# Performance work log

Hardware: AMD Instinct MI355X
Metric: run time of the kernel (lower is better)

## Reference

```python
import jax, jax.numpy as jnp
import numpy as np

DIM = 256
NUM_HEADS = 8
HEAD_DIM = DIM // NUM_HEADS


def setup_inputs() -> dict:
    key = jax.random.key(0)
    k_x, k_wq, k_bq, k_wp, k_bp = jax.random.split(key, 5)
    B, C, H, W = 2, DIM, 48, 48
    x = jax.random.normal(k_x, (B, C, H, W), dtype=jnp.float32)
    # 1x1 convs are pointwise matmuls: store weights as [out, in]
    w_qkv = jax.random.normal(k_wq, (3 * C, C), dtype=jnp.float32) * (1.0 / np.sqrt(C))
    b_qkv = jax.random.normal(k_bq, (3 * C,), dtype=jnp.float32) * 0.01
    w_proj = jax.random.normal(k_wp, (C, C), dtype=jnp.float32) * (1.0 / np.sqrt(C))
    b_proj = jax.random.normal(k_bp, (C,), dtype=jnp.float32) * 0.01
    return {"x": x, "w_qkv": w_qkv, "b_qkv": b_qkv, "w_proj": w_proj, "b_proj": b_proj}


def reference(x, w_qkv, b_qkv, w_proj, b_proj):
    B, C, H, W = x.shape
    N = H * W
    # qkv 1x1 conv -> pointwise channel matmul
    qkv = jnp.einsum('bchw,oc->bohw', x, w_qkv) + b_qkv[None, :, None, None]
    q, k, v = jnp.split(qkv, 3, axis=1)  # each [B, C, H, W]
    q = q.reshape(B, NUM_HEADS, HEAD_DIM, N)
    k = k.reshape(B, NUM_HEADS, HEAD_DIM, N)
    v = v.reshape(B, NUM_HEADS, HEAD_DIM, N)
    scale = 1.0 / (HEAD_DIM ** 0.5)
    attn = jnp.einsum('bhdn,bhdm->bhnm', q, k) * scale  # [B, H, N, N]
    attn = jax.nn.softmax(attn, axis=-1)
    out = jnp.einsum('bhnm,bhdm->bhdn', attn, v)  # [B, heads, head_dim, N]
    out = out.reshape(B, C, H, W)
    out = jnp.einsum('bchw,oc->bohw', out, w_proj) + b_proj[None, :, None, None]
    return out + x
```

## Files before the change

### kernel.cpp

```cpp
#include <hip/hip_runtime.h>
#include <math.h>

#define C_DIM 256
#define NH 8
#define HD 32
#define NPIX 2304
#define NGRP 144
#define TK 64
#define TPB 18

typedef __attribute__((ext_vector_type(8))) short bf16x8;
typedef __attribute__((ext_vector_type(4))) float f32x4;

#define OFF_XT  0u
#define OFF_Q   1179648u
#define OFF_K   2359296u
#define OFF_V   3538944u
#define OFF_OT  4718592u
#define OFF_WQ  5898240u
#define OFF_WP  6094848u
#define OFF_F32 6160384u

__device__ __forceinline__ unsigned short f2b(float f) {
    union { float f; unsigned int u; } c; c.f = f;
    unsigned int u = c.u + 0x7FFFu + ((c.u >> 16) & 1u);
    return (unsigned short)(u >> 16);
}
__device__ __forceinline__ unsigned int pk2(float lo, float hi) {
    union { float f; unsigned int u; } a, b;
    a.f = lo; b.f = hi;
    return __builtin_amdgcn_perm(b.u + 0x8000u, a.u + 0x8000u, 0x07060302u);
}

__global__ __launch_bounds__(256) void prep_all(
        const float* __restrict__ x, const float* __restrict__ wqkv,
        const float* __restrict__ wproj, unsigned short* __restrict__ wsp)
{
    __shared__ unsigned short t_s[64][72];
    const int tid = threadIdx.x;
    const int u = blockIdx.x;
    if (u < 288) {
        const int n0 = (u % 36) * 64, cb = (u / 36) % 4, b = u / 144;
        const int c0 = cb * 64;
        const int nl = tid & 63, cq = tid >> 6;
        #pragma unroll
        for (int p = 0; p < 8; ++p) {
            const int c = p * 8 + cq * 2;
            const float f0 = x[((size_t)b * C_DIM + c0 + c) * NPIX + n0 + nl];
            const float f1 = x[((size_t)b * C_DIM + c0 + c + 1) * NPIX + n0 + nl];
            *(unsigned int*)&t_s[nl][c] = pk2(f0, f1);
        }
        __syncthreads();
        unsigned short* xT = wsp + OFF_XT;
        const int row = tid >> 2, jq = tid & 3;
        #pragma unroll
        for (int hh = 0; hh < 2; ++hh) {
            const int jl = jq * 2 + hh;
            const int jg = cb * 8 + jl;
            const int ngrp = (u % 36) * 4 + (row >> 4);
            unsigned short* dst = xT + (((size_t)b * NGRP + ngrp) * 32 + jg) * 128 + (row & 15) * 8;
            *(uint4*)dst = *(uint4*)&t_s[row][jl * 8];
        }
    } else {
        const int t = (u - 288) * 256 + tid;
        const float* src; unsigned short* dst;
        if (t < 24576) {
            const int m = t >> 5, j = t & 31;
            src = wqkv + ((size_t)m * C_DIM + j * 8);
            dst = wsp + OFF_WQ + ((size_t)((m >> 4) * 32 + j) * 16 + (m & 15)) * 8;
        } else {
            const int t2 = t - 24576, m = t2 >> 5, j = t2 & 31;
            src = wproj + ((size_t)m * C_DIM + j * 8);
            dst = wsp + OFF_WP + ((size_t)((m >> 4) * 32 + j) * 16 + (m & 15)) * 8;
        }
        const float4 f0 = *(const float4*)src, f1 = *(const float4*)(src + 4);
        *(uint4*)dst = make_uint4(pk2(f0.x, f0.y), pk2(f0.z, f0.w),
                                  pk2(f1.x, f1.y), pk2(f1.z, f1.w));
    }
}

__global__ __launch_bounds__(256, 2) void qkv_gemm(
        const unsigned short* __restrict__ xT, const unsigned short* __restrict__ wq,
        const float* __restrict__ bias,
        unsigned short* __restrict__ Qg, unsigned short* __restrict__ Kg,
        unsigned short* __restrict__ Vg)
{
    __shared__ unsigned short eplds[4][2560];
    const int tid = threadIdx.x, wv = tid >> 6, lane = tid & 63;
    const int l15 = lane & 15, quad = lane >> 4;
    const int n0 = blockIdx.x * 256, my = blockIdx.y, b = blockIdx.z;
    const int nw = n0 + wv * 64;

    bf16x8 af[2][8];
    #pragma unroll
    for (int mt = 0; mt < 2; ++mt)
        #pragma unroll
        for (int kc = 0; kc < 8; ++kc)
            af[mt][kc] = *(const bf16x8*)(wq +
                ((size_t)((my * 2 + mt) * 32 + kc * 4 + quad) * 16 + l15) * 8);

    f32x4 acc[2][4];
    #pragma unroll
    for (int mt = 0; mt < 2; ++mt)
        #pragma unroll
        for (int s = 0; s < 4; ++s) acc[mt][s] = (f32x4){0.f, 0.f, 0.f, 0.f};

    #pragma unroll
    for (int sub = 0; sub < 4; ++sub) {
        const int ngrp = (nw + sub * 16) >> 4;
        const unsigned short* bp = xT + ((size_t)b * NGRP + ngrp) * 32 * 128;
        #pragma unroll
        for (int kc = 0; kc < 8; ++kc) {
            const bf16x8 bf = *(const bf16x8*)(bp + (size_t)(kc * 4 + quad) * 128 + l15 * 8);
            acc[0][sub] = __builtin_amdgcn_mfma_f32_16x16x32_bf16(af[0][kc], bf, acc[0][sub], 0, 0, 0);
            acc[1][sub] = __builtin_amdgcn_mfma_f32_16x16x32_bf16(af[1][kc], bf, acc[1][sub], 0, 0, 0);
        }
    }

    const int which = my >> 3;
    const int h = my & 7, bh = b * NH + h;
    float4 b4[2];
    b4[0] = *(const float4*)(bias + my * 32 + quad * 4);
    b4[1] = *(const float4*)(bias + my * 32 + 16 + quad * 4);
    unsigned short* wl = eplds[wv];

    if (which < 2) {
        const float sc = (which == 0) ? 0.25503484f : 1.0f;
        #pragma unroll
        for (int mt = 0; mt < 2; ++mt)
            #pragma unroll
            for (int sub = 0; sub < 4; ++sub) {
                const float v0 = (acc[mt][sub][0] + b4[mt].x) * sc;
                const float v1 = (acc[mt][sub][1] + b4[mt].y) * sc;
                const float v2 = (acc[mt][sub][2] + b4[mt].z) * sc;
                const float v3 = (acc[mt][sub][3] + b4[mt].w) * sc;
                *(uint2*)&wl[(sub * 16 + l15) * 40 + mt * 16 + quad * 4] =
                    make_uint2(pk2(v0, v1), pk2(v2, v3));
            }
        unsigned short* dst = ((which == 0) ? Qg : Kg)
                            + ((size_t)bh * NPIX + nw + lane) * HD;
        #pragma unroll
        for (int i = 0; i < 4; ++i)
            *((uint4*)dst + i) = *(uint4*)&wl[lane * 40 + i * 8];
    } else {
        #pragma unroll
        for (int mt = 0; mt < 2; ++mt)
            #pragma unroll
            for (int sub = 0; sub < 4; ++sub) {
                wl[(mt * 16 + quad * 4 + 0) * 72 + sub * 16 + l15] = f2b(acc[mt][sub][0] + b4[mt].x);
                wl[(mt * 16 + quad * 4 + 1) * 72 + sub * 16 + l15] = f2b(acc[mt][sub][1] + b4[mt].y);
                wl[(mt * 16 + quad * 4 + 2) * 72 + sub * 16 + l15] = f2b(acc[mt][sub][2] + b4[mt].z);
                wl[(mt * 16 + quad * 4 + 3) * 72 + sub * 16 + l15] = f2b(acc[mt][sub][3] + b4[mt].w);
            }
        const int row = lane >> 1, seg = (lane & 1) * 32;
        unsigned short* dst = Vg + ((size_t)bh * HD + row) * NPIX + nw + seg;
        #pragma unroll
        for (int i = 0; i < 4; ++i)
            *((uint4*)dst + i) = *(uint4*)&wl[row * 72 + seg + i * 8];
    }
}

__global__ __launch_bounds__(256, 4) void attn_kernel(
        const unsigned short* __restrict__ Qg, const unsigned short* __restrict__ Kg,
        const unsigned short* __restrict__ Vg,
        float* __restrict__ OtP, float* __restrict__ lsumP)
{
    __shared__ unsigned short k_s[2][TK][40];
    __shared__ unsigned short v_s[2][HD][76];
    __shared__ unsigned short p_s[4][16][76];

    const int tid  = threadIdx.x;
    const int wv   = tid >> 6;
    const int lane = tid & 63;
    const int l15  = lane & 15;
    const int quad = lane >> 4;
    const int bh   = blockIdx.x;
    const int q0   = blockIdx.y * 64;
    const int sp   = blockIdx.z;
    const int t0   = sp * TPB;

    const unsigned short* Qh = Qg + (size_t)bh * NPIX * HD;
    const unsigned short* Kh = Kg + (size_t)bh * NPIX * HD;
    const unsigned short* Vh = Vg + (size_t)bh * HD * NPIX;

    const bf16x8 q_frag = *(const bf16x8*)(Qh + (size_t)(q0 + wv * 16 + l15) * HD + quad * 8);

    const int kr = tid >> 2, kc = (tid & 3) * 8;
    const int vd = tid >> 3, vc = (tid & 7) * 8;

    uint4 kreg = *(const uint4*)(Kh + (size_t)(t0 * TK + kr) * HD + kc);
    uint4 vreg = *(const uint4*)(Vh + (size_t)vd * NPIX + t0 * TK + vc);
    *(uint4*)&k_s[0][kr][kc] = kreg;
    *(uint4*)&v_s[0][vd][vc] = vreg;

    f32x4 o0 = {0.f, 0.f, 0.f, 0.f};
    f32x4 o1 = {0.f, 0.f, 0.f, 0.f};
    float lsum = 0.f;

    for (int t = 0; t < TPB; ++t) {
        const int cur = t & 1;
        if (t + 1 < TPB) {
            const int k0 = (t0 + t + 1) * TK;
            kreg = *(const uint4*)(Kh + (size_t)(k0 + kr) * HD + kc);
            vreg = *(const uint4*)(Vh + (size_t)vd * NPIX + k0 + vc);
        }
        __syncthreads();

        f32x4 s[4];
        #pragma unroll
        for (int kg = 0; kg < 4; ++kg) {
            const bf16x8 kf = *(const bf16x8*)&k_s[cur][kg * 16 + l15][quad * 8];
            s[kg] = __builtin_amdgcn_mfma_f32_16x16x32_bf16(kf, q_frag,
                        (f32x4){0.f, 0.f, 0.f, 0.f}, 0, 0, 0);
        }

        #pragma unroll
        for (int kg = 0; kg < 4; ++kg) {
            const float p0 = exp2f(s[kg][0]);
            const float p1 = exp2f(s[kg][1]);
            const float p2 = exp2f(s[kg][2]);
            const float p3 = exp2f(s[kg][3]);
            lsum += (p0 + p1) + (p2 + p3);
            *(uint2*)&p_s[wv][l15][kg * 16 + quad * 4] =
                make_uint2(pk2(p0, p1), pk2(p2, p3));
        }

        #pragma unroll
        for (int kc2 = 0; kc2 < 2; ++kc2) {
            const bf16x8 pf  = *(const bf16x8*)&p_s[wv][l15][kc2 * 32 + quad * 8];
            const bf16x8 vf0 = *(const bf16x8*)&v_s[cur][l15][kc2 * 32 + quad * 8];
            const bf16x8 vf1 = *(const bf16x8*)&v_s[cur][16 + l15][kc2 * 32 + quad * 8];
            o0 = __builtin_amdgcn_mfma_f32_16x16x32_bf16(vf0, pf, o0, 0, 0, 0);
            o1 = __builtin_amdgcn_mfma_f32_16x16x32_bf16(vf1, pf, o1, 0, 0, 0);
        }

        if (t + 1 < TPB) {
            *(uint4*)&k_s[cur ^ 1][kr][kc] = kreg;
            *(uint4*)&v_s[cur ^ 1][vd][vc] = vreg;
        }
    }

    lsum += __shfl_xor(lsum, 16, 64);
    lsum += __shfl_xor(lsum, 32, 64);

    __syncthreads();
    float* pp = (float*)&p_s[wv][0][0];
    #pragma unroll
    for (int r = 0; r < 4; ++r) {
        pp[l15 * 36 + quad * 4 + r]      = o0[r];
        pp[l15 * 36 + 16 + quad * 4 + r] = o1[r];
    }
    if (quad == 0)
        lsumP[((size_t)sp * 16 + bh) * NPIX + q0 + wv * 16 + l15] = lsum;
    __syncthreads();
    const int q = lane >> 2, off = (lane & 3) * 8;
    float* dst = OtP + (((size_t)sp * 16 + bh) * NPIX + q0 + wv * 16 + q) * 32 + off;
    *(float4*)dst       = *(float4*)&pp[q * 36 + off];
    *((float4*)dst + 1) = *(float4*)&pp[q * 36 + off + 4];
}

__global__ __launch_bounds__(256) void norm_kernel(
        const float* __restrict__ OtP, const float* __restrict__ lsumP,
        unsigned short* __restrict__ OtT)
{
    const int bh = blockIdx.x;
    const int q = blockIdx.y * 256 + threadIdx.x;
    const float* pa = OtP + ((size_t)bh * NPIX + q) * 32;
    const float* pb = OtP + ((size_t)(16 + bh) * NPIX + q) * 32;
    const float inv = 1.f / (lsumP[(size_t)bh * NPIX + q] +
                             lsumP[(size_t)(16 + bh) * NPIX + q]);
    const int b = bh >> 3, h = bh & 7;
    unsigned short* cell = OtT + (((size_t)b * NGRP + (q >> 4)) * 32 + h * 4) * 128
                         + (q & 15) * 8;
    #pragma unroll
    for (int jq = 0; jq < 4; ++jq) {
        const float4 a0 = *(const float4*)(pa + jq * 8);
        const float4 a1 = *(const float4*)(pa + jq * 8 + 4);
        const float4 b0 = *(const float4*)(pb + jq * 8);
        const float4 b1 = *(const float4*)(pb + jq * 8 + 4);
        const float o0 = (a0.x + b0.x) * inv, o1 = (a0.y + b0.y) * inv;
        const float o2 = (a0.z + b0.z) * inv, o3 = (a0.w + b0.w) * inv;
        const float o4 = (a1.x + b1.x) * inv, o5 = (a1.y + b1.y) * inv;
        const float o6 = (a1.z + b1.z) * inv, o7 = (a1.w + b1.w) * inv;
        *(uint4*)(cell + jq * 128) = make_uint4(pk2(o0, o1), pk2(o2, o3),
                                                pk2(o4, o5), pk2(o6, o7));
    }
}

__global__ __launch_bounds__(256) void proj_gemm(
        const unsigned short* __restrict__ OtT, const unsigned short* __restrict__ wp,
        const float* __restrict__ bias, const float* __restrict__ x,
        float* __restrict__ out)
{
    __shared__ float plds[4][576];
    const int tid = threadIdx.x, wv = tid >> 6, lane = tid & 63;
    const int l15 = lane & 15, quad = lane >> 4;
    const int n0 = blockIdx.x * 128, my = blockIdx.y, b = blockIdx.z;
    const int nw = n0 + wv * 32;

    bf16x8 af[8];
    #pragma unroll
    for (int kc = 0; kc < 8; ++kc)
        af[kc] = *(const bf16x8*)(wp + ((size_t)(my * 32 + kc * 4 + quad) * 16 + l15) * 8);

    f32x4 acc[2];
    acc[0] = (f32x4){0.f, 0.f, 0.f, 0.f};
    acc[1] = (f32x4){0.f, 0.f, 0.f, 0.f};

    #pragma unroll
    for (int sub = 0; sub < 2; ++sub) {
        const int ngrp = (nw >> 4) + sub;
        const unsigned short* bp = OtT + ((size_t)b * NGRP + ngrp) * 32 * 128;
        #pragma unroll
        for (int kc = 0; kc < 8; ++kc) {
            const bf16x8 bf = *(const bf16x8*)(bp + (size_t)(kc * 4 + quad) * 128 + l15 * 8);
            acc[sub] = __builtin_amdgcn_mfma_f32_16x16x32_bf16(af[kc], bf, acc[sub], 0, 0, 0);
        }
    }

    float* wl = plds[wv];
    #pragma unroll
    for (int sub = 0; sub < 2; ++sub) {
        wl[(quad * 4 + 0) * 36 + sub * 16 + l15] = acc[sub][0];
        wl[(quad * 4 + 1) * 36 + sub * 16 + l15] = acc[sub][1];
        wl[(quad * 4 + 2) * 36 + sub * 16 + l15] = acc[sub][2];
        wl[(quad * 4 + 3) * 36 + sub * 16 + l15] = acc[sub][3];
    }
    __syncthreads();
    const int m0 = my * 16;
    #pragma unroll
    for (int p = 0; p < 2; ++p) {
        const int row = p * 8 + (lane >> 3), cn = (lane & 7) * 4;
        const int c = m0 + row;
        const size_t idx = ((size_t)b * C_DIM + c) * NPIX + nw + cn;
        const f32x4 v = *(const f32x4*)&wl[row * 36 + cn];
        const f32x4 r = *(const f32x4*)(x + idx);
        const float bv = bias[c];
        f32x4 o;
        o[0] = v[0] + bv + r[0]; o[1] = v[1] + bv + r[1];
        o[2] = v[2] + bv + r[2]; o[3] = v[3] + bv + r[3];
        *(f32x4*)(out + idx) = o;
    }
}

extern "C" void kernel_launch(void* const* d_in, const int* in_sizes, int n_in,
                              void* d_out, int out_size, void* d_ws, size_t ws_size,
                              hipStream_t stream)
{
    const float* x      = (const float*)d_in[0];
    const float* w_qkv  = (const float*)d_in[1];
    const float* b_qkv  = (const float*)d_in[2];
    const float* w_proj = (const float*)d_in[3];
    const float* b_proj = (const float*)d_in[4];
    float* out = (float*)d_out;

    unsigned short* ws = (unsigned short*)d_ws;
    unsigned short* xT  = ws + OFF_XT;
    unsigned short* Qg  = ws + OFF_Q;
    unsigned short* Kg  = ws + OFF_K;
    unsigned short* Vg  = ws + OFF_V;
    unsigned short* OtT = ws + OFF_OT;
    unsigned short* wq  = ws + OFF_WQ;
    unsigned short* wp  = ws + OFF_WP;
    float* fws   = (float*)(ws + OFF_F32);
    float* OtP   = fws;
    float* lsumP = fws + 4718592;

    prep_all<<<dim3(416), 256, 0, stream>>>(x, w_qkv, w_proj, ws);
    qkv_gemm<<<dim3(9, 24, 2), 256, 0, stream>>>(xT, wq, b_qkv, Qg, Kg, Vg);
    attn_kernel<<<dim3(16, 36, 2), 256, 0, stream>>>(Qg, Kg, Vg, OtP, lsumP);
    norm_kernel<<<dim3(16, 9), 256, 0, stream>>>(OtP, lsumP, OtT);
    proj_gemm<<<dim3(18, 16, 2), 256, 0, stream>>>(OtT, wp, b_proj, x, out);
}
```

Measured before the change: 122.6 us.

## Restructure attention: per-wave direct K/V fragment loads, 32 queries per wave, 4-way key split

The attention kernel stops staging K and V through double-buffered shared memory with block barriers. Each wave now loads MFMA fragments directly from global memory, and V gets a new fragment-major layout written by the QKV GEMM so those loads are contiguous. Each wave now covers 32 queries, so every loaded K/V fragment feeds twice as many MFMAs. The key dimension is split four ways instead of two, and the normalization kernel sums four partials. This removes barriers and LDS traffic in the inner loop, but doubles the fp32 partial-output writes and reads and depends on caches to serve the repeated K/V loads.

```diff
diff --git a/kernel.cpp b/kernel.cpp
--- a/kernel.cpp
+++ b/kernel.cpp
@@ -6,8 +6,8 @@
 #define HD 32
 #define NPIX 2304
 #define NGRP 144
-#define TK 64
-#define TPB 18
+#define NSP 4
+#define ATPB 9
 
 typedef __attribute__((ext_vector_type(8))) short bf16x8;
 typedef __attribute__((ext_vector_type(4))) float f32x4;
@@ -83,7 +83,7 @@
         const unsigned short* __restrict__ xT, const unsigned short* __restrict__ wq,
         const float* __restrict__ bias,
         unsigned short* __restrict__ Qg, unsigned short* __restrict__ Kg,
-        unsigned short* __restrict__ Vg)
+        unsigned short* __restrict__ Vfm)
 {
     __shared__ unsigned short eplds[4][2560];
     const int tid = threadIdx.x, wv = tid >> 6, lane = tid & 63;
@@ -152,111 +152,102 @@
                 wl[(mt * 16 + quad * 4 + 2) * 72 + sub * 16 + l15] = f2b(acc[mt][sub][2] + b4[mt].z);
                 wl[(mt * 16 + quad * 4 + 3) * 72 + sub * 16 + l15] = f2b(acc[mt][sub][3] + b4[mt].w);
             }
-        const int row = lane >> 1, seg = (lane & 1) * 32;
-        unsigned short* dst = Vg + ((size_t)bh * HD + row) * NPIX + nw + seg;
+        const int row = lane >> 1;
+        const int half = lane & 1;
+        unsigned short* dst = Vfm + (((size_t)bh * 72 + (nw >> 5) + half) * 2 + (row >> 4)) * 512
+                            + (row & 15) * 32;
         #pragma unroll
         for (int i = 0; i < 4; ++i)
-            *((uint4*)dst + i) = *(uint4*)&wl[row * 72 + seg + i * 8];
+            *((uint4*)dst + i) = *(uint4*)&wl[row * 72 + half * 32 + i * 8];
     }
 }
 
 __global__ __launch_bounds__(256, 4) void attn_kernel(
         const unsigned short* __restrict__ Qg, const unsigned short* __restrict__ Kg,
-        const unsigned short* __restrict__ Vg,
+        const unsigned short* __restrict__ Vfm,
         float* __restrict__ OtP, float* __restrict__ lsumP)
 {
-    __shared__ unsigned short k_s[2][TK][40];
-    __shared__ unsigned short v_s[2][HD][76];
-    __shared__ unsigned short p_s[4][16][76];
-
-    const int tid  = threadIdx.x;
-    const int wv   = tid >> 6;
-    const int lane = tid & 63;
-    const int l15  = lane & 15;
-    const int quad = lane >> 4;
-    const int bh   = blockIdx.x;
-    const int q0   = blockIdx.y * 64;
-    const int sp   = blockIdx.z;
-    const int t0   = sp * TPB;
+    __shared__ unsigned short ps_all[4][2304];
+    const int tid = threadIdx.x, wv = tid >> 6, lane = tid & 63;
+    const int l15 = lane & 15, quad = lane >> 4;
+    const int bh = blockIdx.x, qb = blockIdx.y, sp = blockIdx.z;
+    const int tqb = qb * 128 + wv * 32;
 
     const unsigned short* Qh = Qg + (size_t)bh * NPIX * HD;
     const unsigned short* Kh = Kg + (size_t)bh * NPIX * HD;
-    const unsigned short* Vh = Vg + (size_t)bh * HD * NPIX;
-
-    const bf16x8 q_frag = *(const bf16x8*)(Qh + (size_t)(q0 + wv * 16 + l15) * HD + quad * 8);
-
-    const int kr = tid >> 2, kc = (tid & 3) * 8;
-    const int vd = tid >> 3, vc = (tid & 7) * 8;
-
-    uint4 kreg = *(const uint4*)(Kh + (size_t)(t0 * TK + kr) * HD + kc);
-    uint4 vreg = *(const uint4*)(Vh + (size_t)vd * NPIX + t0 * TK + vc);
-    *(uint4*)&k_s[0][kr][kc] = kreg;
-    *(uint4*)&v_s[0][vd][vc] = vreg;
-
-    f32x4 o0 = {0.f, 0.f, 0.f, 0.f};
-    f32x4 o1 = {0.f, 0.f, 0.f, 0.f};
-    float lsum = 0.f;
-
-    for (int t = 0; t < TPB; ++t) {
-        const int cur = t & 1;
-        if (t + 1 < TPB) {
-            const int k0 = (t0 + t + 1) * TK;
-            kreg = *(const uint4*)(Kh + (size_t)(k0 + kr) * HD + kc);
-            vreg = *(const uint4*)(Vh + (size_t)vd * NPIX + k0 + vc);
-        }
-        __syncthreads();
-
-        f32x4 s[4];
+    const unsigned short* Vb = Vfm + (size_t)bh * 73728;
+
+    const bf16x8 qf0 = *(const bf16x8*)(Qh + (size_t)(tqb + l15) * HD + quad * 8);
+    const bf16x8 qf1 = *(const bf16x8*)(Qh + (size_t)(tqb + 16 + l15) * HD + quad * 8);
+
+    unsigned short* ps = ps_all[wv];
+    f32x4 o[2][2];
+    #pragma unroll
+    for (int i = 0; i < 2; ++i) { o[i][0] = (f32x4){0,0,0,0}; o[i][1] = (f32x4){0,0,0,0}; }
+    float ls0 = 0.f, ls1 = 0.f;
+
+    for (int t = 0; t < ATPB; ++t) {
+        const int k0 = (sp * ATPB + t) * 64;
+        bf16x8 kf[4];
+        #pragma unroll
+        for (int kg = 0; kg < 4; ++kg)
+            kf[kg] = *(const bf16x8*)(Kh + (size_t)(k0 + kg * 16 + l15) * HD + quad * 8);
+        f32x4 s0[4], s1[4];
         #pragma unroll
         for (int kg = 0; kg < 4; ++kg) {
-            const bf16x8 kf = *(const bf16x8*)&k_s[cur][kg * 16 + l15][quad * 8];
-            s[kg] = __builtin_amdgcn_mfma_f32_16x16x32_bf16(kf, q_frag,
-                        (f32x4){0.f, 0.f, 0.f, 0.f}, 0, 0, 0);
-        }
-
+            s0[kg] = __builtin_amdgcn_mfma_f32_16x16x32_bf16(kf[kg], qf0, (f32x4){0,0,0,0}, 0, 0, 0);
+            s1[kg] = __builtin_amdgcn_mfma_f32_16x16x32_bf16(kf[kg], qf1, (f32x4){0,0,0,0}, 0, 0, 0);
+        }
         #pragma unroll
         for (int kg = 0; kg < 4; ++kg) {
-            const float p0 = exp2f(s[kg][0]);
-            const float p1 = exp2f(s[kg][1]);
-            const float p2 = exp2f(s[kg][2]);
-            const float p3 = exp2f(s[kg][3]);
-            lsum += (p0 + p1) + (p2 + p3);
-            *(uint2*)&p_s[wv][l15][kg * 16 + quad * 4] =
-                make_uint2(pk2(p0, p1), pk2(p2, p3));
-        }
-
+            const float a0 = exp2f(s0[kg][0]), a1 = exp2f(s0[kg][1]);
+            const float a2 = exp2f(s0[kg][2]), a3 = exp2f(s0[kg][3]);
+            ls0 += (a0 + a1) + (a2 + a3);
+            *(uint2*)&ps[(size_t)l15 * 72 + kg * 16 + quad * 4] =
+                make_uint2(pk2(a0, a1), pk2(a2, a3));
+            const float b0 = exp2f(s1[kg][0]), b1 = exp2f(s1[kg][1]);
+            const float b2 = exp2f(s1[kg][2]), b3 = exp2f(s1[kg][3]);
+            ls1 += (b0 + b1) + (b2 + b3);
+            *(uint2*)&ps[(size_t)(16 + l15) * 72 + kg * 16 + quad * 4] =
+                make_uint2(pk2(b0, b1), pk2(b2, b3));
+        }
         #pragma unroll
         for (int kc2 = 0; kc2 < 2; ++kc2) {
-            const bf16x8 pf  = *(const bf16x8*)&p_s[wv][l15][kc2 * 32 + quad * 8];
-            const bf16x8 vf0 = *(const bf16x8*)&v_s[cur][l15][kc2 * 32 + quad * 8];
-            const bf16x8 vf1 = *(const bf16x8*)&v_s[cur][16 + l15][kc2 * 32 + quad * 8];
-            o0 = __builtin_amdgcn_mfma_f32_16x16x32_bf16(vf0, pf, o0, 0, 0, 0);
-            o1 = __builtin_amdgcn_mfma_f32_16x16x32_bf16(vf1, pf, o1, 0, 0, 0);
-        }
-
-        if (t + 1 < TPB) {
-            *(uint4*)&k_s[cur ^ 1][kr][kc] = kreg;
-            *(uint4*)&v_s[cur ^ 1][vd][vc] = vreg;
-        }
-    }
-
-    lsum += __shfl_xor(lsum, 16, 64);
-    lsum += __shfl_xor(lsum, 32, 64);
-
-    __syncthreads();
-    float* pp = (float*)&p_s[wv][0][0];
-    #pragma unroll
-    for (int r = 0; r < 4; ++r) {
-        pp[l15 * 36 + quad * 4 + r]      = o0[r];
-        pp[l15 * 36 + 16 + quad * 4 + r] = o1[r];
-    }
-    if (quad == 0)
-        lsumP[((size_t)sp * 16 + bh) * NPIX + q0 + wv * 16 + l15] = lsum;
-    __syncthreads();
-    const int q = lane >> 2, off = (lane & 3) * 8;
-    float* dst = OtP + (((size_t)sp * 16 + bh) * NPIX + q0 + wv * 16 + q) * 32 + off;
-    *(float4*)dst       = *(float4*)&pp[q * 36 + off];
-    *((float4*)dst + 1) = *(float4*)&pp[q * 36 + off + 4];
+            const int kb = (k0 >> 5) + kc2;
+            const bf16x8 vf0 = *(const bf16x8*)(Vb + ((size_t)kb * 2 + 0) * 512 + l15 * 32 + quad * 8);
+            const bf16x8 vf1 = *(const bf16x8*)(Vb + ((size_t)kb * 2 + 1) * 512 + l15 * 32 + quad * 8);
+            const bf16x8 pf0 = *(const bf16x8*)&ps[(size_t)l15 * 72 + kc2 * 32 + quad * 8];
+            const bf16x8 pf1 = *(const bf16x8*)&ps[(size_t)(16 + l15) * 72 + kc2 * 32 + quad * 8];
+            o[0][0] = __builtin_amdgcn_mfma_f32_16x16x32_bf16(vf0, pf0, o[0][0], 0, 0, 0);
+            o[0][1] = __builtin_amdgcn_mfma_f32_16x16x32_bf16(vf1, pf0, o[0][1], 0, 0, 0);
+            o[1][0] = __builtin_amdgcn_mfma_f32_16x16x32_bf16(vf0, pf1, o[1][0], 0, 0, 0);
+            o[1][1] = __builtin_amdgcn_mfma_f32_16x16x32_bf16(vf1, pf1, o[1][1], 0, 0, 0);
+        }
+    }
+
+    ls0 += __shfl_xor(ls0, 16, 64); ls0 += __shfl_xor(ls0, 32, 64);
+    ls1 += __shfl_xor(ls1, 16, 64); ls1 += __shfl_xor(ls1, 32, 64);
+    if (quad == 0) {
+        lsumP[((size_t)sp * 16 + bh) * NPIX + tqb + l15]      = ls0;
+        lsumP[((size_t)sp * 16 + bh) * NPIX + tqb + 16 + l15] = ls1;
+    }
+
+    float* tl = (float*)ps;
+    #pragma unroll
+    for (int qs = 0; qs < 2; ++qs) {
+        __builtin_amdgcn_s_waitcnt(0);
+        #pragma unroll
+        for (int r = 0; r < 4; ++r) {
+            tl[l15 * 36 + quad * 4 + r]      = o[qs][0][r];
+            tl[l15 * 36 + 16 + quad * 4 + r] = o[qs][1][r];
+        }
+        __builtin_amdgcn_s_waitcnt(0);
+        const int qq = lane >> 2, j = lane & 3;
+        float* dst = OtP + (((size_t)sp * 16 + bh) * NPIX + tqb + qs * 16 + qq) * 32 + j * 8;
+        *(float4*)dst       = *(float4*)&tl[qq * 36 + j * 8];
+        *((float4*)dst + 1) = *(float4*)&tl[qq * 36 + j * 8 + 4];
+        __builtin_amdgcn_s_waitcnt(0);
+    }
 }
 
 __global__ __launch_bounds__(256) void norm_kernel(
@@ -265,25 +256,25 @@
 {
     const int bh = blockIdx.x;
     const int q = blockIdx.y * 256 + threadIdx.x;
-    const float* pa = OtP + ((size_t)bh * NPIX + q) * 32;
-    const float* pb = OtP + ((size_t)(16 + bh) * NPIX + q) * 32;
+    const float* p0 = OtP + ((size_t)bh * NPIX + q) * 32;
+    const float* p1 = OtP + ((size_t)(16 + bh) * NPIX + q) * 32;
+    const float* p2 = OtP + ((size_t)(32 + bh) * NPIX + q) * 32;
+    const float* p3 = OtP + ((size_t)(48 + bh) * NPIX + q) * 32;
     const float inv = 1.f / (lsumP[(size_t)bh * NPIX + q] +
-                             lsumP[(size_t)(16 + bh) * NPIX + q]);
+                             lsumP[(size_t)(16 + bh) * NPIX + q] +
+                             lsumP[(size_t)(32 + bh) * NPIX + q] +
+                             lsumP[(size_t)(48 + bh) * NPIX + q]);
     const int b = bh >> 3, h = bh & 7;
     unsigned short* cell = OtT + (((size_t)b * NGRP + (q >> 4)) * 32 + h * 4) * 128
                          + (q & 15) * 8;
     #pragma unroll
     for (int jq = 0; jq < 4; ++jq) {
-        const float4 a0 = *(const float4*)(pa + jq * 8);
-        const float4 a1 = *(const float4*)(pa + jq * 8 + 4);
-        const float4 b0 = *(const float4*)(pb + jq * 8);
-        const float4 b1 = *(const float4*)(pb + jq * 8 + 4);
-        const float o0 = (a0.x + b0.x) * inv, o1 = (a0.y + b0.y) * inv;
-        const float o2 = (a0.z + b0.z) * inv, o3 = (a0.w + b0.w) * inv;
-        const float o4 = (a1.x + b1.x) * inv, o5 = (a1.y + b1.y) * inv;
-        const float o6 = (a1.z + b1.z) * inv, o7 = (a1.w + b1.w) * inv;
-        *(uint4*)(cell + jq * 128) = make_uint4(pk2(o0, o1), pk2(o2, o3),
-                                                pk2(o4, o5), pk2(o6, o7));
+        float v[8];
+        #pragma unroll
+        for (int e = 0; e < 8; ++e)
+            v[e] = (p0[jq * 8 + e] + p1[jq * 8 + e] + p2[jq * 8 + e] + p3[jq * 8 + e]) * inv;
+        *(uint4*)(cell + jq * 128) = make_uint4(pk2(v[0], v[1]), pk2(v[2], v[3]),
+                                                pk2(v[4], v[5]), pk2(v[6], v[7]));
     }
 }
 
@@ -358,17 +349,17 @@
     unsigned short* xT  = ws + OFF_XT;
     unsigned short* Qg  = ws + OFF_Q;
     unsigned short* Kg  = ws + OFF_K;
-    unsigned short* Vg  = ws + OFF_V;
+    unsigned short* Vfm = ws + OFF_V;
     unsigned short* OtT = ws + OFF_OT;
     unsigned short* wq  = ws + OFF_WQ;
     unsigned short* wp  = ws + OFF_WP;
     float* fws   = (float*)(ws + OFF_F32);
     float* OtP   = fws;
-    float* lsumP = fws + 4718592;
+    float* lsumP = fws + 9437184;
 
     prep_all<<<dim3(416), 256, 0, stream>>>(x, w_qkv, w_proj, ws);
-    qkv_gemm<<<dim3(9, 24, 2), 256, 0, stream>>>(xT, wq, b_qkv, Qg, Kg, Vg);
-    attn_kernel<<<dim3(16, 36, 2), 256, 0, stream>>>(Qg, Kg, Vg, OtP, lsumP);
+    qkv_gemm<<<dim3(9, 24, 2), 256, 0, stream>>>(xT, wq, b_qkv, Qg, Kg, Vfm);
+    attn_kernel<<<dim3(16, 18, 4), 256, 0, stream>>>(Qg, Kg, Vfm, OtP, lsumP);
     norm_kernel<<<dim3(16, 9), 256, 0, stream>>>(OtP, lsumP, OtT);
     proj_gemm<<<dim3(18, 16, 2), 256, 0, stream>>>(OtT, wp, b_proj, x, out);
 }
```

Result: slower. 125.8 us (+2.5%).
